# Performance work log

Hardware: AMD Instinct MI355X
Metric: run time of the kernel (lower is better)

The kernel has to match this reference:

```python
import jax, jax.numpy as jnp
import numpy as np

B, C, H, W_SP = 16, 128, 28, 28
F, KS, STRIDE, PAD = 128, 3, 1, 1
CHUNK = 4      # filters per chunk for the L1 reduction (limits intermediate size)
EPS = 1e-12


def setup_inputs() -> dict:
    key = jax.random.key(0)
    kx, kw = jax.random.split(key)
    x = jax.random.normal(kx, (B, C, H, W_SP), dtype=jnp.float32)
    # kaiming_normal_: std = sqrt(2 / fan_in), fan_in = C*KS*KS
    std = float(np.sqrt(2.0 / (C * KS * KS)))
    W = jax.random.normal(kw, (F, C, KS, KS), dtype=jnp.float32) * std
    return {"x": x, "W": W}


def _patches(x):
    # im2col: [B, C*KS*KS, h_out, w_out], feature order (c, kh, kw) like torch unfold
    p = jax.lax.conv_general_dilated_patches(
        x, (KS, KS), (STRIDE, STRIDE), [(PAD, PAD), (PAD, PAD)],
        dimension_numbers=('NCHW', 'OIHW', 'NCHW'))
    b, k, ho, wo = p.shape
    return p.reshape(b, k, ho * wo), ho, wo


def reference(x, W):
    P, ho, wo = _patches(x)          # [B, K, L]
    Wc = W.reshape(F, -1)            # [F, K]
    K = Wc.shape[1]

    # Forward value: out = -cdist_L1(W, X_col) = -sum_k |W[f,k] - P[b,k,l]|
    # computed in filter chunks to avoid the full [F, K, B*L] diff tensor.
    Wch = Wc.reshape(F // CHUNK, CHUNK, K)
    def chunk_fn(wc):                # wc: [CHUNK, K]
        return jnp.sum(jnp.abs(wc[None, :, :, None] - P[:, None, :, :]), axis=2)  # [B, CHUNK, L]
    neg_l1 = -jax.lax.map(chunk_fn, Wch)                     # [F//CHUNK, B, CHUNK, L]
    neg_l1 = jnp.transpose(neg_l1, (1, 0, 2, 3)).reshape(P.shape[0], F, -1)  # [B, F, L]

    # Gradient path in original (straight-through): -cdist_L2, via GEMM decomposition.
    d2 = (jnp.sum(Wc * Wc, axis=1)[None, :, None]
          + jnp.sum(P * P, axis=1)[:, None, :]
          - 2.0 * jnp.einsum('fk,bkl->bfl', Wc, P))
    neg_l2 = -jnp.sqrt(jnp.maximum(d2, EPS))

    # value = -L1, gradient flows through -L2 (out.data = out_2.data in torch)
    out = neg_l2 + jax.lax.stop_gradient(neg_l1 - neg_l2)    # [B, F, L]
    return out.reshape(P.shape[0], F, ho, wo)
```

## Files before the change

kernel.cpp:

```cpp
#include <hip/hip_runtime.h>


#define B_    16
#define C_    128
#define HH    28
#define WW    28
#define F_    128
#define L_    (HH * WW)
#define K_    (C_ * 9)
#define M_    (B_ * L_)
#define TM    64
#define BC    8
#define KC    (BC * 9)
#define KP    (KC / 2)
#define SLAB  (B_ * F_ * L_)
#define NMT   (M_ / TM)
#define QS    4096.0f
#define QB    32768.5f

__device__ __forceinline__ unsigned sad16(unsigned a, unsigned b, unsigned c) {
    asm("v_sad_u16 %0, %1, %2, %0" : "+v"(c) : "v"(a), "v"(b));
    return c;
}

__global__ __launch_bounds__(256, 4)
void adder2d_main(const float* __restrict__ x, const float* __restrict__ Wg,
                  float* __restrict__ dst, int nch, int direct) {
    __shared__ __align__(16) unsigned Plq[KP][TM];
    __shared__ __align__(16) unsigned Wlq[KP][F_];

    const int t    = threadIdx.x;
    const int lane = t & 63;
    const int w    = t >> 6;
    const int tx   = lane & 7;
    const int ty   = lane >> 3;
    const int fw   = 32 * w;
    const int mt   = blockIdx.x, sp = blockIdx.z;
    const int c0   = sp * nch * BC;

    const int m  = mt * TM + lane;
    const int b  = m / L_;
    const int l  = m - b * L_;
    const int ho = l / WW, wo = l - ho * WW;
    int   toff[9];
    float sc[9];
    #pragma unroll
    for (int r = 0; r < 9; ++r) {
        const int dy = r / 3 - 1;
        const int dx = r - (r / 3) * 3 - 1;
        const bool ok = ((unsigned)(ho + dy) < (unsigned)HH) &&
                        ((unsigned)(wo + dx) < (unsigned)WW);
        toff[r] = ok ? (dy * WW + dx) : 0;
        sc[r]   = ok ? QS : 0.0f;
    }
    const float* xb = x + (size_t)b * (C_ * L_) + l;

    const int pb = (w & 1) + 4 * (w >> 1);
    const int fW = t >> 1;
    const int pW = t & 1;
    const float* wbase = Wg + (size_t)fW * K_;

    unsigned acc[8][4];
    #pragma unroll
    for (int i = 0; i < 8; ++i)
        #pragma unroll
        for (int j = 0; j < 4; ++j) acc[i][j] = 0u;

    float ppre[18];
    auto loadP = [&](int c8) {
        const float* x1 = xb + (size_t)(c8 + pb) * L_;
        const float* x2 = x1 + 2 * L_;
        #pragma unroll
        for (int r = 0; r < 9; ++r) {
            ppre[r]     = x1[toff[r]];
            ppre[9 + r] = x2[toff[r]];
        }
    };

    loadP(c0);

    #pragma unroll 1
    for (int ch = 0; ch < nch; ++ch) {
        const int c8 = c0 + ch * BC;
        #pragma unroll
        for (int r = 0; r < 9; ++r) {
            const unsigned qlo = (unsigned)__builtin_fmaf(ppre[r],     sc[r], QB);
            const unsigned qhi = (unsigned)__builtin_fmaf(ppre[9 + r], sc[r], QB);
            Plq[w * 9 + r][lane] = (qlo & 0xffffu) | (qhi << 16);
        }
        #pragma unroll
        for (int s = 0; s < 2; ++s) {
            const float* w1 = wbase + (size_t)(c8 + pW + 4 * s) * 9;
            #pragma unroll
            for (int i = 0; i < 9; ++i) {
                const unsigned qlo = (unsigned)__builtin_fmaf(w1[i],      QS, QB);
                const unsigned qhi = (unsigned)__builtin_fmaf(w1[i + 18], QS, QB);
                Wlq[(pW + 2 * s) * 9 + i][fW] = (qlo & 0xffffu) | (qhi << 16);
            }
        }
        if (ch + 1 < nch) loadP(c8 + BC);
        asm volatile("s_waitcnt lgkmcnt(0)" ::: "memory");
        __builtin_amdgcn_s_barrier();
        asm volatile("" ::: "memory");
        __builtin_amdgcn_sched_barrier(0);
        #pragma unroll 6
        for (int kp = 0; kp < KP; ++kp) {
            const uint4 pA = *(const uint4*)&Plq[kp][tx * 8];
            const uint4 pB = *(const uint4*)&Plq[kp][tx * 8 + 4];
            const uint4 wA = *(const uint4*)&Wlq[kp][fw + ty * 4];
            const unsigned pm[8] = {pA.x, pA.y, pA.z, pA.w,
                                    pB.x, pB.y, pB.z, pB.w};
            const unsigned wn[4] = {wA.x, wA.y, wA.z, wA.w};
            #pragma unroll
            for (int i = 0; i < 8; ++i)
                #pragma unroll
                for (int j = 0; j < 4; ++j)
                    acc[i][j] = sad16(pm[i], wn[j], acc[i][j]);
        }
        if (ch + 1 < nch) {
            asm volatile("" ::: "memory");
            __builtin_amdgcn_sched_barrier(0);
            __builtin_amdgcn_s_barrier();
            asm volatile("" ::: "memory");
        }
    }

    const int mb = mt * TM + tx * 8;
    const int bI = mb / L_;
    const int lb = mb - bI * L_;
    float* slab = direct ? dst : dst + (size_t)sp * SLAB;
    const float qs = (direct ? -1.0f : 1.0f) / QS;
    #pragma unroll
    for (int j = 0; j < 4; ++j) {
        const int f = fw + ty * 4 + j;
        float* o = &slab[(size_t)(bI * F_ + f) * L_ + lb];
        *(float4*)o       = make_float4(qs * (float)acc[0][j], qs * (float)acc[1][j],
                                        qs * (float)acc[2][j], qs * (float)acc[3][j]);
        *(float4*)(o + 4) = make_float4(qs * (float)acc[4][j], qs * (float)acc[5][j],
                                        qs * (float)acc[6][j], qs * (float)acc[7][j]);
    }
}

__global__ __launch_bounds__(256)
void adder2d_combine(const float* __restrict__ ws, float* __restrict__ out,
                     int nslab) {
    const int i = blockIdx.x * 256 + threadIdx.x;
    float4 r = make_float4(0.0f, 0.0f, 0.0f, 0.0f);
    for (int s = 0; s < nslab; ++s) {
        const float4 p = ((const float4*)(ws + (size_t)s * SLAB))[i];
        r.x += p.x; r.y += p.y; r.z += p.z; r.w += p.w;
    }
    ((float4*)out)[i] = make_float4(-r.x, -r.y, -r.z, -r.w);
}

extern "C" void kernel_launch(void* const* d_in, const int* in_sizes, int n_in,
                              void* d_out, int out_size, void* d_ws, size_t ws_size,
                              hipStream_t stream) {
    const float* x = (const float*)d_in[0];
    const float* W = (const float*)d_in[1];
    float* out = (float*)d_out;
    float* ws  = (float*)d_ws;

    const int nsp = 4;
    if (ws_size >= (size_t)nsp * SLAB * sizeof(float)) {
        dim3 grid(NMT, 1, nsp);
        adder2d_main<<<grid, 256, 0, stream>>>(x, W, ws, (C_ / BC) / nsp, 0);
        adder2d_combine<<<SLAB / 4 / 256, 256, 0, stream>>>(ws, out, nsp);
    } else {
        dim3 grid(NMT, 1, 1);
        adder2d_main<<<grid, 256, 0, stream>>>(x, W, out, C_ / BC, 1);
    }
}
```

Measured before the change: 114.3 us.

## Use 128x128 block tile with 8x8 per-thread SAD accumulators and split-K of 8

Doubles the spatial tile per block from 64 to 128 and gives each thread an 8x8 accumulator tile instead of 8x4. This raises data reuse per LDS read in the v_sad_u16 inner loop. The split over channels grows from 4 to 8 slabs, so the grid keeps the same block count, and the occupancy hint drops to 2 blocks per CU. The register prefetch of the next channel chunk is removed. The cost is twice the workspace write and combine traffic, lower occupancy, and global-load latency that is no longer hidden behind the SAD loop.

```diff
diff --git a/kernel.cpp b/kernel.cpp
--- a/kernel.cpp
+++ b/kernel.cpp
@@ -9,12 +9,14 @@
 #define L_    (HH * WW)
 #define K_    (C_ * 9)
 #define M_    (B_ * L_)
-#define TM    64
+#define TM    128
 #define BC    8
 #define KC    (BC * 9)
 #define KP    (KC / 2)
+#define NMT   (M_ / TM)
+#define NSP   8
+#define NCH   ((C_ / BC) / NSP)
 #define SLAB  (B_ * F_ * L_)
-#define NMT   (M_ / TM)
 #define QS    4096.0f
 #define QB    32768.5f
 
@@ -23,7 +25,7 @@
     return c;
 }
 
-__global__ __launch_bounds__(256, 4)
+__global__ __launch_bounds__(256, 2)
 void adder2d_main(const float* __restrict__ x, const float* __restrict__ Wg,
                   float* __restrict__ dst, int nch, int direct) {
     __shared__ __align__(16) unsigned Plq[KP][TM];
@@ -34,87 +36,83 @@
     const int w    = t >> 6;
     const int tx   = lane & 7;
     const int ty   = lane >> 3;
-    const int fw   = 32 * w;
+    const int mh   = w >> 1;
+    const int fh   = w & 1;
     const int mt   = blockIdx.x, sp = blockIdx.z;
-    const int c0   = sp * nch * BC;
+    const int c0   = sp * NCH * BC;
 
-    const int m  = mt * TM + lane;
-    const int b  = m / L_;
-    const int l  = m - b * L_;
-    const int ho = l / WW, wo = l - ho * WW;
+    const int mcs = t & 127;
+    const int g   = t >> 7;
+    const int ms  = mt * TM + mcs;
+    const int bs  = ms / L_;
+    const int ls  = ms - bs * L_;
+    const int hos = ls / WW, wos = ls - (ls / WW) * WW;
     int   toff[9];
     float sc[9];
     #pragma unroll
     for (int r = 0; r < 9; ++r) {
         const int dy = r / 3 - 1;
         const int dx = r - (r / 3) * 3 - 1;
-        const bool ok = ((unsigned)(ho + dy) < (unsigned)HH) &&
-                        ((unsigned)(wo + dx) < (unsigned)WW);
+        const bool ok = ((unsigned)(hos + dy) < (unsigned)HH) &&
+                        ((unsigned)(wos + dx) < (unsigned)WW);
         toff[r] = ok ? (dy * WW + dx) : 0;
         sc[r]   = ok ? QS : 0.0f;
     }
-    const float* xb = x + (size_t)b * (C_ * L_) + l;
+    const float* xbs = x + (size_t)bs * (C_ * L_) + ls;
+    const float* wrow = Wg + (size_t)mcs * K_;
 
-    const int pb = (w & 1) + 4 * (w >> 1);
-    const int fW = t >> 1;
-    const int pW = t & 1;
-    const float* wbase = Wg + (size_t)fW * K_;
-
-    unsigned acc[8][4];
+    unsigned acc[8][8];
     #pragma unroll
     for (int i = 0; i < 8; ++i)
         #pragma unroll
-        for (int j = 0; j < 4; ++j) acc[i][j] = 0u;
-
-    float ppre[18];
-    auto loadP = [&](int c8) {
-        const float* x1 = xb + (size_t)(c8 + pb) * L_;
-        const float* x2 = x1 + 2 * L_;
-        #pragma unroll
-        for (int r = 0; r < 9; ++r) {
-            ppre[r]     = x1[toff[r]];
-            ppre[9 + r] = x2[toff[r]];
-        }
-    };
-
-    loadP(c0);
+        for (int j = 0; j < 8; ++j) acc[i][j] = 0u;
 
     #pragma unroll 1
     for (int ch = 0; ch < nch; ++ch) {
         const int c8 = c0 + ch * BC;
         #pragma unroll
-        for (int r = 0; r < 9; ++r) {
-            const unsigned qlo = (unsigned)__builtin_fmaf(ppre[r],     sc[r], QB);
-            const unsigned qhi = (unsigned)__builtin_fmaf(ppre[9 + r], sc[r], QB);
-            Plq[w * 9 + r][lane] = (qlo & 0xffffu) | (qhi << 16);
+        for (int pp = 0; pp < 2; ++pp) {
+            const int pr = 2 * g + pp;
+            const int lo = (pr & 1) + 4 * (pr >> 1);
+            const float* x1 = xbs + (size_t)(c8 + lo) * L_;
+            const float* x2 = x1 + 2 * L_;
+            #pragma unroll
+            for (int r = 0; r < 9; ++r) {
+                const unsigned qlo = (unsigned)__builtin_fmaf(x1[toff[r]], sc[r], QB);
+                const unsigned qhi = (unsigned)__builtin_fmaf(x2[toff[r]], sc[r], QB);
+                Plq[pr * 9 + r][mcs] = (qlo & 0xffffu) | (qhi << 16);
+            }
         }
         #pragma unroll
-        for (int s = 0; s < 2; ++s) {
-            const float* w1 = wbase + (size_t)(c8 + pW + 4 * s) * 9;
+        for (int pp = 0; pp < 2; ++pp) {
+            const int pr = 2 * g + pp;
+            const int lo = (pr & 1) + 4 * (pr >> 1);
+            const float* w1 = wrow + (size_t)(c8 + lo) * 9;
             #pragma unroll
-            for (int i = 0; i < 9; ++i) {
-                const unsigned qlo = (unsigned)__builtin_fmaf(w1[i],      QS, QB);
-                const unsigned qhi = (unsigned)__builtin_fmaf(w1[i + 18], QS, QB);
-                Wlq[(pW + 2 * s) * 9 + i][fW] = (qlo & 0xffffu) | (qhi << 16);
+            for (int r = 0; r < 9; ++r) {
+                const unsigned qlo = (unsigned)__builtin_fmaf(w1[r],      QS, QB);
+                const unsigned qhi = (unsigned)__builtin_fmaf(w1[r + 18], QS, QB);
+                Wlq[pr * 9 + r][mcs] = (qlo & 0xffffu) | (qhi << 16);
             }
         }
-        if (ch + 1 < nch) loadP(c8 + BC);
         asm volatile("s_waitcnt lgkmcnt(0)" ::: "memory");
         __builtin_amdgcn_s_barrier();
         asm volatile("" ::: "memory");
         __builtin_amdgcn_sched_barrier(0);
-        #pragma unroll 6
+        #pragma unroll 4
         for (int kp = 0; kp < KP; ++kp) {
-            const uint4 pA = *(const uint4*)&Plq[kp][tx * 8];
-            const uint4 pB = *(const uint4*)&Plq[kp][tx * 8 + 4];
-            const uint4 wA = *(const uint4*)&Wlq[kp][fw + ty * 4];
+            const uint4 pA = *(const uint4*)&Plq[kp][mh * 64 + tx * 8];
+            const uint4 pB = *(const uint4*)&Plq[kp][mh * 64 + tx * 8 + 4];
+            const uint4 wA = *(const uint4*)&Wlq[kp][fh * 64 + ty * 8];
+            const uint4 wB = *(const uint4*)&Wlq[kp][fh * 64 + ty * 8 + 4];
             const unsigned pm[8] = {pA.x, pA.y, pA.z, pA.w,
                                     pB.x, pB.y, pB.z, pB.w};
-            const unsigned wn[4] = {wA.x, wA.y, wA.z, wA.w};
+            const unsigned wn[8] = {wA.x, wA.y, wA.z, wA.w,
+                                    wB.x, wB.y, wB.z, wB.w};
             #pragma unroll
             for (int i = 0; i < 8; ++i)
                 #pragma unroll
-                for (int j = 0; j < 4; ++j)
+                for (int j = 0; j < 8; ++j)
                     acc[i][j] = sad16(pm[i], wn[j], acc[i][j]);
         }
         if (ch + 1 < nch) {
@@ -125,14 +123,14 @@
         }
     }
 
-    const int mb = mt * TM + tx * 8;
+    const int mb = mt * TM + mh * 64 + tx * 8;
     const int bI = mb / L_;
     const int lb = mb - bI * L_;
     float* slab = direct ? dst : dst + (size_t)sp * SLAB;
     const float qs = (direct ? -1.0f : 1.0f) / QS;
     #pragma unroll
-    for (int j = 0; j < 4; ++j) {
-        const int f = fw + ty * 4 + j;
+    for (int j = 0; j < 8; ++j) {
+        const int f = fh * 64 + ty * 8 + j;
         float* o = &slab[(size_t)(bI * F_ + f) * L_ + lb];
         *(float4*)o       = make_float4(qs * (float)acc[0][j], qs * (float)acc[1][j],
                                         qs * (float)acc[2][j], qs * (float)acc[3][j]);
@@ -161,11 +159,10 @@
     float* out = (float*)d_out;
     float* ws  = (float*)d_ws;
 
-    const int nsp = 4;
-    if (ws_size >= (size_t)nsp * SLAB * sizeof(float)) {
-        dim3 grid(NMT, 1, nsp);
-        adder2d_main<<<grid, 256, 0, stream>>>(x, W, ws, (C_ / BC) / nsp, 0);
-        adder2d_combine<<<SLAB / 4 / 256, 256, 0, stream>>>(ws, out, nsp);
+    if (ws_size >= (size_t)NSP * SLAB * sizeof(float)) {
+        dim3 grid(NMT, 1, NSP);
+        adder2d_main<<<grid, 256, 0, stream>>>(x, W, ws, NCH, 0);
+        adder2d_combine<<<SLAB / 4 / 256, 256, 0, stream>>>(ws, out, NSP);
     } else {
         dim3 grid(NMT, 1, 1);
         adder2d_main<<<grid, 256, 0, stream>>>(x, W, out, C_ / BC, 1);
```

New measurement: 120.6 us. 5.5% more time.
